# Performance work log

Hardware: AMD Instinct MI355X
Metric: run time of the kernel (lower is better)

Reference implementation:

```python
import jax, jax.numpy as jnp
import numpy as np

B, S, D, H = 4, 2048, 1024, 16
DH = D // H  # 64
R = 12       # random-projection rank forced by U's view()
EPS = 1e-6


def setup_inputs() -> dict:
    key = jax.random.key(0)
    ks = jax.random.split(key, 8)
    sc = 1.0 / np.sqrt(D)
    return {
        "Q": jax.random.normal(ks[0], (B, S, D), jnp.float32),
        "K": jax.random.normal(ks[1], (B, S, D), jnp.float32),
        "V": jax.random.normal(ks[2], (B, S, D), jnp.float32),
        "U": jax.random.normal(ks[3], (B, H, R, DH), jnp.float32),
        "W_Q": jax.random.normal(ks[4], (D, D), jnp.float32) * sc,
        "W_K": jax.random.normal(ks[5], (D, D), jnp.float32) * sc,
        "W_V": jax.random.normal(ks[6], (D, D), jnp.float32) * sc,
        "W_lin": jax.random.normal(ks[7], (D, D), jnp.float32) * sc,
        "b_lin": jnp.zeros((D,), jnp.float32),
        "gamma": jnp.ones((D,), jnp.float32),
        "beta": jnp.zeros((D,), jnp.float32),
    }


def reference(Q, K, V, U, W_Q, W_K, W_V, W_lin, b_lin, gamma, beta):
    b, s, d_model = Q.shape

    def proj(X, W):  # nn.Linear (no bias): X @ W^T, split heads -> [B,H,S,dh]
        return (X @ W.T).reshape(b, s, H, DH).transpose(0, 2, 1, 3)

    q = proj(Q, W_Q)
    k = proj(K, W_K)
    v = proj(V, W_V)

    # scores = (q @ U^T)^T @ k : random projection onto R=12 dims
    s1 = jnp.einsum('bhsd,bhrd->bhsr', q, U)          # [B,H,S,R]
    s2 = jnp.einsum('bhsr,bhsd->bhrd', s1, k)         # [B,H,R,dh]
    attn = jax.nn.softmax(s2, axis=-1)                # softmax over dh
    ctx = jnp.einsum('bhrd,bhsd->bhrs', attn, v)      # [B,H,R,S]
    # transpose(1,2) -> [B,R,H,S], flatten to [B, R*H*S/D, D]
    ctx = ctx.transpose(0, 2, 1, 3).reshape(b, -1, d_model)

    out = ctx @ W_lin.T + b_lin                       # final linear
    # dropout is identity in eval mode; then LayerNorm(eps=1e-6)
    mu = jnp.mean(out, axis=-1, keepdims=True)
    var = jnp.var(out, axis=-1, keepdims=True)
    return (out - mu) * jax.lax.rsqrt(var + EPS) * gamma + beta
```

## Files before the change

kernel.cpp:

```cpp
#include <hip/hip_runtime.h>

#define NB 4
#define NS 2048
#define ND 1024
#define NH 16
#define NDH 64
#define NR 12
#define NRH 192

typedef __attribute__((ext_vector_type(8))) short bf16x8;
typedef __attribute__((ext_vector_type(4))) float f32x4;

__device__ __forceinline__ unsigned short rnbf(float f) {
  unsigned u = __float_as_uint(f);
  u += 0x7fffu + ((u >> 16) & 1u);
  return (unsigned short)(u >> 16);
}
__device__ __forceinline__ float bf2f(unsigned short h) {
  return __uint_as_float(((unsigned)h) << 16);
}

__device__ __forceinline__ unsigned cvtpk(float a, float b) {
  unsigned r;
  asm("v_cvt_pk_bf16_f32 %0, %1, %2" : "=v"(r) : "v"(a), "v"(b));
  return r;
}
__device__ __forceinline__ uint4 pk_hi(float4 u, float4 w) {
  uint4 h;
  h.x = cvtpk(u.x, u.y); h.y = cvtpk(u.z, u.w);
  h.z = cvtpk(w.x, w.y); h.w = cvtpk(w.z, w.w);
  return h;
}
__device__ __forceinline__ unsigned lo2(float a, float b, unsigned hh) {
  float ah = __uint_as_float(hh << 16);
  float bh = __uint_as_float(hh & 0xffff0000u);
  return cvtpk(a - ah, b - bh);
}
__device__ __forceinline__ uint4 pk_lo(float4 u, float4 w, uint4 h) {
  uint4 l;
  l.x = lo2(u.x, u.y, h.x); l.y = lo2(u.z, u.w, h.y);
  l.z = lo2(w.x, w.y, h.z); l.w = lo2(w.z, w.w, h.w);
  return l;
}

__device__ __forceinline__ void gload16(const void* g, void* l) {
  __builtin_amdgcn_global_load_lds(
      (const __attribute__((address_space(1))) unsigned int*)g,
      (__attribute__((address_space(3))) unsigned int*)l, 16, 0, 0);
}

#define MFMA(a, b, c) __builtin_amdgcn_mfma_f32_16x16x32_bf16(a, b, c, 0, 0, 0)

__global__ __launch_bounds__(256) void build_wqeff(const float* __restrict__ U,
                                                   const float* __restrict__ WQ,
                                                   unsigned short* __restrict__ wqhi,
                                                   unsigned short* __restrict__ wqlo) {
  int idx = blockIdx.x;
  int hr = idx % (NH * NR);
  int h = hr / NR;
  __shared__ float u[NDH];
  int t = threadIdx.x;
  if (t < NDH) u[t] = U[(size_t)idx * NDH + t];
  __syncthreads();
  int e0 = t * 4;
  float a0 = 0.f, a1 = 0.f, a2 = 0.f, a3 = 0.f;
  const float* wbase = WQ + (size_t)h * NDH * ND + e0;
#pragma unroll 4
  for (int d = 0; d < NDH; ++d) {
    float uv = u[d];
    const float* wr = wbase + (size_t)d * ND;
    a0 += uv * wr[0]; a1 += uv * wr[1]; a2 += uv * wr[2]; a3 += uv * wr[3];
  }
  ushort4 h4, l4;
  h4.x = rnbf(a0); l4.x = rnbf(a0 - bf2f(h4.x));
  h4.y = rnbf(a1); l4.y = rnbf(a1 - bf2f(h4.y));
  h4.z = rnbf(a2); l4.z = rnbf(a2 - bf2f(h4.z));
  h4.w = rnbf(a3); l4.w = rnbf(a3 - bf2f(h4.w));
  *(ushort4*)&wqhi[(size_t)idx * ND + e0] = h4;
  *(ushort4*)&wqlo[(size_t)idx * ND + e0] = l4;
}

template <bool PAIR>
__global__ __launch_bounds__(256) void gemm_tn(
    const float* __restrict__ Af,
    const unsigned short* __restrict__ Bhi, const unsigned short* __restrict__ Blo,
    unsigned short* __restrict__ C0, unsigned short* __restrict__ C1) {
  constexpr int NBUF = PAIR ? 2 : 1;
  __shared__ unsigned short As[2][NBUF][32 * 64];
  __shared__ unsigned short Bs[2][NBUF][64 * 64];
  const int tid = threadIdx.x;
  const int lane = tid & 63;
  const int wid = tid >> 6;
  const int wm = wid >> 1, wn = wid & 1;

  int lin = blockIdx.x;
  int xcd = lin & 7, slot = lin >> 3;
  int b = slot / 24;
  int rem = slot % 24;
  int m0 = ((rem / 3) * 8 + xcd) * 32;
  int n0 = (rem % 3) * 64;

  const float* pA = Af + (size_t)b * NS * ND;
  const unsigned short* pBhi = Bhi + (size_t)b * NRH * ND;
  const unsigned short* pBlo = PAIR ? Blo + (size_t)b * NRH * ND : nullptr;

  const int rsub = lane >> 3;
  const int slotg = (lane & 7) ^ rsub;
  const int arow = tid >> 3;
  const int jg = tid & 7;

  f32x4 acc[2];
  acc[0] = (f32x4){0.f, 0.f, 0.f, 0.f};
  acc[1] = (f32x4){0.f, 0.f, 0.f, 0.f};

  {
    const float* asrc = pA + (size_t)(m0 + arow) * ND + jg * 8;
    float4 au = *(const float4*)(asrc);
    float4 av = *(const float4*)(asrc + 4);
#pragma unroll
    for (int cc = 0; cc < 2; ++cc) {
      int c = wid * 2 + cc;
      int grow = n0 + c * 8 + rsub;
      gload16(&pBhi[(size_t)grow * ND + slotg * 8], &Bs[0][0][c * 512]);
      if (PAIR)
        gload16(&pBlo[(size_t)grow * ND + slotg * 8], &Bs[0][NBUF - 1][c * 512]);
    }
    uint4 h = pk_hi(au, av);
    char* dst = (char*)&As[0][0][0] + arow * 128 + ((jg ^ (arow & 7)) << 4);
    *(uint4*)dst = h;
    if (PAIR) *(uint4*)(dst + 4096) = pk_lo(au, av, h);
  }
  __syncthreads();

  int p = 0;
  for (int k0 = 0; k0 < ND; k0 += 64, p ^= 1) {
    const bool pre = (k0 + 64) < ND;
    float4 aun = {}, avn = {};
    if (pre) {
      const float* asrc = pA + (size_t)(m0 + arow) * ND + k0 + 64 + jg * 8;
      aun = *(const float4*)(asrc);
      avn = *(const float4*)(asrc + 4);
#pragma unroll
      for (int cc = 0; cc < 2; ++cc) {
        int c = wid * 2 + cc;
        int grow = n0 + c * 8 + rsub;
        gload16(&pBhi[(size_t)grow * ND + k0 + 64 + slotg * 8],
                &Bs[p ^ 1][0][c * 512]);
        if (PAIR)
          gload16(&pBlo[(size_t)grow * ND + k0 + 64 + slotg * 8],
                  &Bs[p ^ 1][NBUF - 1][c * 512]);
      }
    }
#pragma unroll
    for (int kk = 0; kk < 64; kk += 32) {
      int sig = (kk >> 3) + (lane >> 4);
      bf16x8 ah, al, bh[2], bl[2];
      {
        int r = wm * 16 + (lane & 15);
        int off = r * 128 + ((sig ^ (r & 7)) << 4);
        ah = *(const bf16x8*)((const char*)&As[p][0][0] + off);
        if (PAIR) al = *(const bf16x8*)((const char*)&As[p][NBUF - 1][0] + off);
      }
#pragma unroll
      for (int fn = 0; fn < 2; ++fn) {
        int r = wn * 32 + fn * 16 + (lane & 15);
        int off = r * 128 + ((sig ^ (r & 7)) << 4);
        bh[fn] = *(const bf16x8*)((const char*)&Bs[p][0][0] + off);
        if (PAIR)
          bl[fn] = *(const bf16x8*)((const char*)&Bs[p][NBUF - 1][0] + off);
      }
#pragma unroll
      for (int fn = 0; fn < 2; ++fn) {
        acc[fn] = MFMA(ah, bh[fn], acc[fn]);
        if (PAIR) {
          acc[fn] = MFMA(ah, bl[fn], acc[fn]);
          acc[fn] = MFMA(al, bh[fn], acc[fn]);
        }
      }
    }
    if (pre) {
      uint4 h = pk_hi(aun, avn);
      char* dst =
          (char*)&As[p ^ 1][0][0] + arow * 128 + ((jg ^ (arow & 7)) << 4);
      *(uint4*)dst = h;
      if (PAIR) *(uint4*)(dst + 4096) = pk_lo(aun, avn, h);
    }
    __syncthreads();
  }

  const int jr = lane >> 4, cl = lane & 15;
#pragma unroll
  for (int fn = 0; fn < 2; ++fn) {
    f32x4 v = acc[fn];
    int s = m0 + wm * 16 + jr * 4;
    int rh = n0 + wn * 32 + fn * 16 + cl;
    int orow = PAIR ? rh : (rh % NR) * NH + rh / NR;
    size_t o = ((size_t)b * NRH + orow) * NS + s;
    ushort4 h4;
    h4.x = rnbf(v[0]); h4.y = rnbf(v[1]);
    h4.z = rnbf(v[2]); h4.w = rnbf(v[3]);
    *(ushort4*)&C0[o] = h4;
    if (PAIR) {
      ushort4 l4;
      l4.x = rnbf(v[0] - bf2f(h4.x)); l4.y = rnbf(v[1] - bf2f(h4.y));
      l4.z = rnbf(v[2] - bf2f(h4.z)); l4.w = rnbf(v[3] - bf2f(h4.w));
      *(ushort4*)&C1[o] = l4;
    }
  }
}

__global__ __launch_bounds__(256) void gemm_g2(
    const unsigned short* __restrict__ Ahi, const unsigned short* __restrict__ Alo,
    const float* __restrict__ Kf, float* __restrict__ P,
    int kchunk, int nz) {
  __shared__ unsigned short As[2][64 * 64];
  __shared__ unsigned short Bs[2][64 * 64];
  __shared__ float tbuf[64 * 68];
  const int tid = threadIdx.x;
  const int lane = tid & 63;
  const int wid = tid >> 6;
  const int wm = wid >> 1, wn = wid & 1;

  int lin = blockIdx.x;
  int bz, m_idx, n_idx;
  if (nz == 16) {
    int xcd = lin & 7, slot = lin >> 3;
    bz = xcd + 8 * (slot / 48);
    int rem = slot % 48;
    m_idx = rem / 16; n_idx = rem % 16;
  } else {
    bz = lin / 48;
    int rem = lin % 48;
    m_idx = rem / 16; n_idx = rem % 16;
  }
  const int m0 = m_idx * 64, n0 = n_idx * 64;
  const int b = bz % NB;
  const int kbeg = (bz / NB) * kchunk;
  const unsigned short* pAhi = Ahi + (size_t)b * NRH * NS;
  const unsigned short* pAlo = Alo + (size_t)b * NRH * NS;
  const float* pK = Kf + (size_t)b * NS * ND;

  const int rsub = lane >> 3;
  const int slotg = (lane & 7) ^ rsub;
  const int sr = tid >> 2;
  const int eg = (tid & 3) * 16;

  f32x4 acc[2][2];
#pragma unroll
  for (int i = 0; i < 2; ++i)
#pragma unroll
    for (int j = 0; j < 2; ++j) acc[i][j] = (f32x4){0.f, 0.f, 0.f, 0.f};

  float4 kr0, kr1, kr2, kr3;
  {
    const float* ksrc = pK + (size_t)(kbeg + sr) * ND + n0 + eg;
    kr0 = *(const float4*)(ksrc + 0);
    kr1 = *(const float4*)(ksrc + 4);
    kr2 = *(const float4*)(ksrc + 8);
    kr3 = *(const float4*)(ksrc + 12);
  }

  for (int k0 = kbeg; k0 < kbeg + kchunk; k0 += 64) {
#pragma unroll
    for (int cc = 0; cc < 2; ++cc) {
      int c = wid * 2 + cc;
      int grow = m0 + c * 8 + rsub;
      gload16(&pAhi[(size_t)grow * NS + k0 + slotg * 8], &As[0][c * 512]);
      gload16(&pAlo[(size_t)grow * NS + k0 + slotg * 8], &As[1][c * 512]);
    }
    {
      float* td = &tbuf[sr * 68 + eg];
      *(float4*)(td + 0) = kr0;
      *(float4*)(td + 4) = kr1;
      *(float4*)(td + 8) = kr2;
      *(float4*)(td + 12) = kr3;
    }
    __syncthreads();
    {
      const int e = tid & 63;
      const int sg = (tid >> 6) * 16;
      float v[16];
#pragma unroll
      for (int i = 0; i < 16; ++i) v[i] = tbuf[(sg + i) * 68 + e];
      float4 u0 = {v[0], v[1], v[2], v[3]},   w0 = {v[4], v[5], v[6], v[7]};
      float4 u1 = {v[8], v[9], v[10], v[11]}, w1 = {v[12], v[13], v[14], v[15]};
      uint4 h0 = pk_hi(u0, w0), h1 = pk_hi(u1, w1);
      int j0 = sg >> 3;
      char* dbase = (char*)&Bs[0][0] + e * 128;
      *(uint4*)(dbase + (((j0 + 0) ^ (e & 7)) << 4)) = h0;
      *(uint4*)(dbase + (((j0 + 1) ^ (e & 7)) << 4)) = h1;
      char* dlo = (char*)&Bs[1][0] + e * 128;
      *(uint4*)(dlo + (((j0 + 0) ^ (e & 7)) << 4)) = pk_lo(u0, w0, h0);
      *(uint4*)(dlo + (((j0 + 1) ^ (e & 7)) << 4)) = pk_lo(u1, w1, h1);
    }
    __syncthreads();
    if (k0 + 64 < kbeg + kchunk) {
      const float* ksrc = pK + (size_t)(k0 + 64 + sr) * ND + n0 + eg;
      kr0 = *(const float4*)(ksrc + 0);
      kr1 = *(const float4*)(ksrc + 4);
      kr2 = *(const float4*)(ksrc + 8);
      kr3 = *(const float4*)(ksrc + 12);
    }
#pragma unroll
    for (int kk = 0; kk < 64; kk += 32) {
      int sig = (kk >> 3) + (lane >> 4);
      bf16x8 ah[2], al[2], bh[2], bl[2];
#pragma unroll
      for (int fm = 0; fm < 2; ++fm) {
        int r = wm * 32 + fm * 16 + (lane & 15);
        int off = r * 128 + ((sig ^ (r & 7)) << 4);
        ah[fm] = *(const bf16x8*)((const char*)&As[0][0] + off);
        al[fm] = *(const bf16x8*)((const char*)&As[1][0] + off);
      }
#pragma unroll
      for (int fn = 0; fn < 2; ++fn) {
        int r = wn * 32 + fn * 16 + (lane & 15);
        int off = r * 128 + ((sig ^ (r & 7)) << 4);
        bh[fn] = *(const bf16x8*)((const char*)&Bs[0][0] + off);
        bl[fn] = *(const bf16x8*)((const char*)&Bs[1][0] + off);
      }
#pragma unroll
      for (int fm = 0; fm < 2; ++fm)
#pragma unroll
        for (int fn = 0; fn < 2; ++fn) {
          acc[fm][fn] = MFMA(ah[fm], bh[fn], acc[fm][fn]);
          acc[fm][fn] = MFMA(ah[fm], bl[fn], acc[fm][fn]);
          acc[fm][fn] = MFMA(al[fm], bh[fn], acc[fm][fn]);
        }
    }
    __syncthreads();
  }

  const int jr = lane >> 4, cl = lane & 15;
  float* pc = P + (size_t)bz * NRH * ND;
#pragma unroll
  for (int fm = 0; fm < 2; ++fm)
#pragma unroll
    for (int fn = 0; fn < 2; ++fn) {
      f32x4 v = acc[fm][fn];
      int gcol = n0 + wn * 32 + fn * 16 + cl;
#pragma unroll
      for (int j = 0; j < 4; ++j) {
        int m = m0 + wm * 32 + fm * 16 + jr * 4 + j;
        pc[(size_t)m * ND + gcol] = v[j];
      }
    }
}

__global__ __launch_bounds__(256) void gemm_g4(
    const unsigned short* __restrict__ A, const float* __restrict__ Bf,
    float* __restrict__ lin) {
  __shared__ unsigned short As[2][64 * 64];
  __shared__ unsigned short Bs[2][64 * 64];
  const int tid = threadIdx.x;
  const int lane = tid & 63;
  const int wid = tid >> 6;
  const int wm = wid >> 1, wn = wid & 1;
  const int m0 = (blockIdx.x >> 4) * 64, n0 = (blockIdx.x & 15) * 64;
  const int rsub = lane >> 3;
  const int slotg = (lane & 7) ^ rsub;
  const int brow = tid >> 2;
  const int jbase = (tid & 3) * 2;

  f32x4 acc[2][2];
#pragma unroll
  for (int i = 0; i < 2; ++i)
#pragma unroll
    for (int j = 0; j < 2; ++j) acc[i][j] = (f32x4){0.f, 0.f, 0.f, 0.f};

#pragma unroll
  for (int cc = 0; cc < 2; ++cc) {
    int c = wid * 2 + cc;
    gload16(&A[(size_t)(m0 + c * 8 + rsub) * ND + slotg * 8], &As[0][c * 512]);
  }
  {
    const float* bsrc = Bf + (size_t)(n0 + brow) * ND + jbase * 8;
    float4 u0 = *(const float4*)(bsrc + 0), v0 = *(const float4*)(bsrc + 4);
    float4 u1 = *(const float4*)(bsrc + 8), v1 = *(const float4*)(bsrc + 12);
    char* dbase = (char*)&Bs[0][0] + brow * 128;
    *(uint4*)(dbase + (((jbase + 0) ^ (brow & 7)) << 4)) = pk_hi(u0, v0);
    *(uint4*)(dbase + (((jbase + 1) ^ (brow & 7)) << 4)) = pk_hi(u1, v1);
  }
  __syncthreads();

  int p = 0;
  for (int k0 = 0; k0 < ND; k0 += 64, p ^= 1) {
    const bool pre = (k0 + 64) < ND;
    float4 pu0 = {}, pv0 = {}, pu1 = {}, pv1 = {};
    if (pre) {
#pragma unroll
      for (int cc = 0; cc < 2; ++cc) {
        int c = wid * 2 + cc;
        gload16(&A[(size_t)(m0 + c * 8 + rsub) * ND + k0 + 64 + slotg * 8],
                &As[p ^ 1][c * 512]);
      }
      const float* bsrc = Bf + (size_t)(n0 + brow) * ND + k0 + 64 + jbase * 8;
      pu0 = *(const float4*)(bsrc + 0); pv0 = *(const float4*)(bsrc + 4);
      pu1 = *(const float4*)(bsrc + 8); pv1 = *(const float4*)(bsrc + 12);
    }
#pragma unroll
    for (int kk = 0; kk < 64; kk += 32) {
      int sig = (kk >> 3) + (lane >> 4);
      bf16x8 ah[2], bh[2];
#pragma unroll
      for (int fm = 0; fm < 2; ++fm) {
        int r = wm * 32 + fm * 16 + (lane & 15);
        int off = r * 128 + ((sig ^ (r & 7)) << 4);
        ah[fm] = *(const bf16x8*)((const char*)&As[p][0] + off);
      }
#pragma unroll
      for (int fn = 0; fn < 2; ++fn) {
        int r = wn * 32 + fn * 16 + (lane & 15);
        int off = r * 128 + ((sig ^ (r & 7)) << 4);
        bh[fn] = *(const bf16x8*)((const char*)&Bs[p][0] + off);
      }
#pragma unroll
      for (int fm = 0; fm < 2; ++fm)
#pragma unroll
        for (int fn = 0; fn < 2; ++fn)
          acc[fm][fn] = MFMA(ah[fm], bh[fn], acc[fm][fn]);
    }
    if (pre) {
      char* dbase = (char*)&Bs[p ^ 1][0] + brow * 128;
      *(uint4*)(dbase + (((jbase + 0) ^ (brow & 7)) << 4)) = pk_hi(pu0, pv0);
      *(uint4*)(dbase + (((jbase + 1) ^ (brow & 7)) << 4)) = pk_hi(pu1, pv1);
    }
    __syncthreads();
  }

  const int jr = lane >> 4, cl = lane & 15;
#pragma unroll
  for (int fm = 0; fm < 2; ++fm)
#pragma unroll
    for (int fn = 0; fn < 2; ++fn) {
      f32x4 v = acc[fm][fn];
      int gcol = n0 + wn * 32 + fn * 16 + cl;
#pragma unroll
      for (int j = 0; j < 4; ++j) {
        int m = m0 + wm * 32 + fm * 16 + jr * 4 + j;
        lin[(size_t)m * ND + gcol] = v[j];
      }
    }
}

__global__ __launch_bounds__(256) void bias_ln(const float* __restrict__ lin,
                                               const float* __restrict__ bias,
                                               const float* __restrict__ gamma,
                                               const float* __restrict__ beta,
                                               float* __restrict__ out) {
  int row = blockIdx.x;
  int t = threadIdx.x;
  float4 a = ((const float4*)(lin + (size_t)row * ND))[t];
  float4 bv = ((const float4*)bias)[t];
  a.x += bv.x; a.y += bv.y; a.z += bv.z; a.w += bv.w;

  float s = a.x + a.y + a.z + a.w;
  float ss = a.x * a.x + a.y * a.y + a.z * a.z + a.w * a.w;
#pragma unroll
  for (int off = 32; off > 0; off >>= 1) {
    s += __shfl_xor(s, off);
    ss += __shfl_xor(ss, off);
  }
  __shared__ float red[8];
  int wave = t >> 6, lane = t & 63;
  if (lane == 0) { red[wave] = s; red[4 + wave] = ss; }
  __syncthreads();
  s = red[0] + red[1] + red[2] + red[3];
  ss = red[4] + red[5] + red[6] + red[7];
  float mu = s * (1.0f / ND);
  float var = ss * (1.0f / ND) - mu * mu;
  float inv = rsqrtf(var + 1e-6f);
  float4 g = ((const float4*)gamma)[t];
  float4 be = ((const float4*)beta)[t];
  float4 o;
  o.x = (a.x - mu) * inv * g.x + be.x;
  o.y = (a.y - mu) * inv * g.y + be.y;
  o.z = (a.z - mu) * inv * g.z + be.z;
  o.w = (a.w - mu) * inv * g.w + be.w;
  ((float4*)(out + (size_t)row * ND))[t] = o;
}

__global__ __launch_bounds__(256) void sm_k(const float* __restrict__ P,
                                            int nsplit,
                                            const float* __restrict__ WK,
                                            const float* __restrict__ WV,
                                            unsigned short* __restrict__ A2) {
  int x = blockIdx.x;
  int xcd = x & 7, within = x >> 3;
  int h = xcd + 8 * (within & 1);
  int rb = within >> 1;
  int r = rb >> 2, b = rb & 3;
  int idx = (b * NH + h) * NR + r;
  int rh = h * NR + r;

  const int t = threadIdx.x;
  const int lane = t & 63, wv = t >> 6;
  __shared__ float t1s[ND];
  __shared__ float s2s[NDH];
  __shared__ float attns[NDH];

  {
    const size_t sstride = (size_t)NB * NRH * ND;
    const float* base = P + ((size_t)b * NRH + rh) * ND;
    float4 a = ((const float4*)base)[t];
    for (int s = 1; s < nsplit; ++s) {
      float4 v = ((const float4*)(base + (size_t)s * sstride))[t];
      a.x += v.x; a.y += v.y; a.z += v.z; a.w += v.w;
    }
    ((float4*)t1s)[t] = a;
  }
  __syncthreads();

  for (int j = 0; j < 16; ++j) {
    int d = wv * 16 + j;
    const float* row = WK + (size_t)(h * NDH + d) * ND;
    float acc = 0.f;
#pragma unroll
    for (int i = 0; i < 16; ++i) acc += row[lane + i * 64] * t1s[lane + i * 64];
#pragma unroll
    for (int off = 32; off > 0; off >>= 1) acc += __shfl_xor(acc, off);
    if (lane == 0) s2s[d] = acc;
  }
  __syncthreads();

  if (t < NDH) {
    float s2 = s2s[t];
    float m = s2;
#pragma unroll
    for (int off = 32; off > 0; off >>= 1) m = fmaxf(m, __shfl_xor(m, off));
    float e = __expf(s2 - m);
    float sum = e;
#pragma unroll
    for (int off = 32; off > 0; off >>= 1) sum += __shfl_xor(sum, off);
    attns[t] = e / sum;
  }
  __syncthreads();

  {
    int e0 = t * 4;
    const float* wvp = WV + (size_t)h * NDH * ND + e0;
    float a0 = 0.f, a1 = 0.f, a2 = 0.f, a3 = 0.f;
#pragma unroll 4
    for (int dd = 0; dd < NDH; ++dd) {
      float4 wvv = *(const float4*)&wvp[(size_t)dd * ND];
      float a = attns[dd];
      a0 += a * wvv.x; a1 += a * wvv.y; a2 += a * wvv.z; a3 += a * wvv.w;
    }
    ushort4 o;
    o.x = rnbf(a0); o.y = rnbf(a1); o.z = rnbf(a2); o.w = rnbf(a3);
    *(ushort4*)&A2[(size_t)idx * ND + e0] = o;
  }
}

extern "C" void kernel_launch(void* const* d_in, const int* in_sizes, int n_in,
                              void* d_out, int out_size, void* d_ws, size_t ws_size,
                              hipStream_t stream) {
  const float* Q = (const float*)d_in[0];
  const float* K = (const float*)d_in[1];
  const float* V = (const float*)d_in[2];
  const float* U = (const float*)d_in[3];
  const float* WQ = (const float*)d_in[4];
  const float* WK = (const float*)d_in[5];
  const float* WV = (const float*)d_in[6];
  const float* WL = (const float*)d_in[7];
  const float* bl = (const float*)d_in[8];
  const float* ga = (const float*)d_in[9];
  const float* be = (const float*)d_in[10];
  float* out = (float*)d_out;
  char* w = (char*)d_ws;

  unsigned short* wqhi = (unsigned short*)w;
  unsigned short* wqlo = (unsigned short*)(w + 1572864);
  unsigned short* A2b = wqhi;
  unsigned short* s1hi = (unsigned short*)(w + 3145728);
  unsigned short* s1lo = (unsigned short*)(w + 6291456);
  unsigned short* ctxb = (unsigned short*)(w + 9437184);
  float* lin = (float*)(w + 12582912);
  float* P = (float*)(w + 18874368);

  size_t avail = ws_size > 18874368 ? ws_size - 18874368 : 0;
  int sG2 = 1;
  while (sG2 * 2 <= 4 && 3145728ull * (size_t)(sG2 * 2) <= avail) sG2 *= 2;

  build_wqeff<<<NB * NH * NR, 256, 0, stream>>>(U, WQ, wqhi, wqlo);

  gemm_tn<true><<<768, 256, 0, stream>>>(Q, wqhi, wqlo, s1hi, s1lo);

  gemm_g2<<<48 * NB * sG2, 256, 0, stream>>>(s1hi, s1lo, K, P, 2048 / sG2,
                                             NB * sG2);

  sm_k<<<NB * NH * NR, 256, 0, stream>>>(P, sG2, WK, WV, A2b);

  gemm_tn<false><<<768, 256, 0, stream>>>(V, A2b, nullptr, ctxb, nullptr);

  gemm_g4<<<384, 256, 0, stream>>>(ctxb, WL, lin);

  bias_ln<<<NB * 384, 256, 0, stream>>>(lin, bl, ga, be, out);
}
```

Measured before the change: 107.7 us.

## Halve GEMM M-tiles and drop LDS double buffering to double grid size

The Q/V projection GEMMs (gemm_tn) shrink their M tile from 32 to 16 rows and the output GEMM (gemm_g4) from 64 to 32 rows, doubling the launch grids. Both kernels drop the register-prefetch/LDS double-buffer pipeline for a single-buffer load, sync, compute, sync loop. The aim is more blocks and less LDS per block for better occupancy and wave coverage across CUs. The cost is that global-load latency is no longer hidden behind MFMA work, B tiles are re-read more often, and there is an odd `&As[0][0] == nullptr ? nullptr : ...` destination expression.

```diff
diff --git a/kernel.cpp b/kernel.cpp
--- a/kernel.cpp
+++ b/kernel.cpp
@@ -86,18 +86,17 @@
     const unsigned short* __restrict__ Bhi, const unsigned short* __restrict__ Blo,
     unsigned short* __restrict__ C0, unsigned short* __restrict__ C1) {
   constexpr int NBUF = PAIR ? 2 : 1;
-  __shared__ unsigned short As[2][NBUF][32 * 64];
-  __shared__ unsigned short Bs[2][NBUF][64 * 64];
+  __shared__ unsigned short As[NBUF][16 * 64];
+  __shared__ unsigned short Bs[NBUF][64 * 64];
   const int tid = threadIdx.x;
   const int lane = tid & 63;
   const int wid = tid >> 6;
-  const int wm = wid >> 1, wn = wid & 1;
 
   int lin = blockIdx.x;
   int xcd = lin & 7, slot = lin >> 3;
-  int b = slot / 24;
-  int rem = slot % 24;
-  int m0 = ((rem / 3) * 8 + xcd) * 32;
+  int b = slot / 48;
+  int rem = slot % 48;
+  int m0 = ((rem / 3) * 8 + xcd) * 16;
   int n0 = (rem % 3) * 64;
 
   const float* pA = Af + (size_t)b * NS * ND;
@@ -106,104 +105,75 @@
 
   const int rsub = lane >> 3;
   const int slotg = (lane & 7) ^ rsub;
-  const int arow = tid >> 3;
-  const int jg = tid & 7;
-
-  f32x4 acc[2];
-  acc[0] = (f32x4){0.f, 0.f, 0.f, 0.f};
-  acc[1] = (f32x4){0.f, 0.f, 0.f, 0.f};
-
-  {
-    const float* asrc = pA + (size_t)(m0 + arow) * ND + jg * 8;
-    float4 au = *(const float4*)(asrc);
-    float4 av = *(const float4*)(asrc + 4);
+  const int arow = tid >> 4;
+  const int aj = (tid & 15) >> 1;
+  const int ah8 = (tid & 1) * 8;
+
+  f32x4 acc = (f32x4){0.f, 0.f, 0.f, 0.f};
+
+  for (int k0 = 0; k0 < ND; k0 += 64) {
+    {
+      const float* asrc = pA + (size_t)(m0 + arow) * ND + k0 + (tid & 15) * 4;
+      float4 v = *(const float4*)asrc;
+      uint2 h;
+      h.x = cvtpk(v.x, v.y); h.y = cvtpk(v.z, v.w);
+      char* dst = (char*)&As[0][0] + arow * 128 + ((aj ^ (arow & 7)) << 4) + ah8;
+      *(uint2*)dst = h;
+      if (PAIR) {
+        uint2 l;
+        l.x = lo2(v.x, v.y, h.x); l.y = lo2(v.z, v.w, h.y);
+        *(uint2*)(dst + 2048) = l;
+      }
+    }
 #pragma unroll
     for (int cc = 0; cc < 2; ++cc) {
       int c = wid * 2 + cc;
       int grow = n0 + c * 8 + rsub;
-      gload16(&pBhi[(size_t)grow * ND + slotg * 8], &Bs[0][0][c * 512]);
+      gload16(&pBhi[(size_t)grow * ND + k0 + slotg * 8], &As[0][0] == nullptr ? nullptr : &Bs[0][c * 512]);
       if (PAIR)
-        gload16(&pBlo[(size_t)grow * ND + slotg * 8], &Bs[0][NBUF - 1][c * 512]);
-    }
-    uint4 h = pk_hi(au, av);
-    char* dst = (char*)&As[0][0][0] + arow * 128 + ((jg ^ (arow & 7)) << 4);
-    *(uint4*)dst = h;
-    if (PAIR) *(uint4*)(dst + 4096) = pk_lo(au, av, h);
-  }
-  __syncthreads();
-
-  int p = 0;
-  for (int k0 = 0; k0 < ND; k0 += 64, p ^= 1) {
-    const bool pre = (k0 + 64) < ND;
-    float4 aun = {}, avn = {};
-    if (pre) {
-      const float* asrc = pA + (size_t)(m0 + arow) * ND + k0 + 64 + jg * 8;
-      aun = *(const float4*)(asrc);
-      avn = *(const float4*)(asrc + 4);
-#pragma unroll
-      for (int cc = 0; cc < 2; ++cc) {
-        int c = wid * 2 + cc;
-        int grow = n0 + c * 8 + rsub;
-        gload16(&pBhi[(size_t)grow * ND + k0 + 64 + slotg * 8],
-                &Bs[p ^ 1][0][c * 512]);
-        if (PAIR)
-          gload16(&pBlo[(size_t)grow * ND + k0 + 64 + slotg * 8],
-                  &Bs[p ^ 1][NBUF - 1][c * 512]);
-      }
-    }
+        gload16(&pBlo[(size_t)grow * ND + k0 + slotg * 8], &Bs[NBUF - 1][c * 512]);
+    }
+    __syncthreads();
+
 #pragma unroll
     for (int kk = 0; kk < 64; kk += 32) {
       int sig = (kk >> 3) + (lane >> 4);
-      bf16x8 ah, al, bh[2], bl[2];
+      bf16x8 ah, al, bh, bl;
       {
-        int r = wm * 16 + (lane & 15);
+        int r = lane & 15;
         int off = r * 128 + ((sig ^ (r & 7)) << 4);
-        ah = *(const bf16x8*)((const char*)&As[p][0][0] + off);
-        if (PAIR) al = *(const bf16x8*)((const char*)&As[p][NBUF - 1][0] + off);
-      }
-#pragma unroll
-      for (int fn = 0; fn < 2; ++fn) {
-        int r = wn * 32 + fn * 16 + (lane & 15);
+        ah = *(const bf16x8*)((const char*)&As[0][0] + off);
+        if (PAIR) al = *(const bf16x8*)((const char*)&As[0][0] + 2048 + off);
+      }
+      {
+        int r = wid * 16 + (lane & 15);
         int off = r * 128 + ((sig ^ (r & 7)) << 4);
-        bh[fn] = *(const bf16x8*)((const char*)&Bs[p][0][0] + off);
-        if (PAIR)
-          bl[fn] = *(const bf16x8*)((const char*)&Bs[p][NBUF - 1][0] + off);
-      }
-#pragma unroll
-      for (int fn = 0; fn < 2; ++fn) {
-        acc[fn] = MFMA(ah, bh[fn], acc[fn]);
-        if (PAIR) {
-          acc[fn] = MFMA(ah, bl[fn], acc[fn]);
-          acc[fn] = MFMA(al, bh[fn], acc[fn]);
-        }
-      }
-    }
-    if (pre) {
-      uint4 h = pk_hi(aun, avn);
-      char* dst =
-          (char*)&As[p ^ 1][0][0] + arow * 128 + ((jg ^ (arow & 7)) << 4);
-      *(uint4*)dst = h;
-      if (PAIR) *(uint4*)(dst + 4096) = pk_lo(aun, avn, h);
+        bh = *(const bf16x8*)((const char*)&Bs[0][0] + off);
+        if (PAIR) bl = *(const bf16x8*)((const char*)&Bs[0][0] + 8192 + off);
+      }
+      acc = MFMA(ah, bh, acc);
+      if (PAIR) {
+        acc = MFMA(ah, bl, acc);
+        acc = MFMA(al, bh, acc);
+      }
     }
     __syncthreads();
   }
 
   const int jr = lane >> 4, cl = lane & 15;
-#pragma unroll
-  for (int fn = 0; fn < 2; ++fn) {
-    f32x4 v = acc[fn];
-    int s = m0 + wm * 16 + jr * 4;
-    int rh = n0 + wn * 32 + fn * 16 + cl;
+  {
+    int s = m0 + jr * 4;
+    int rh = n0 + wid * 16 + cl;
     int orow = PAIR ? rh : (rh % NR) * NH + rh / NR;
     size_t o = ((size_t)b * NRH + orow) * NS + s;
     ushort4 h4;
-    h4.x = rnbf(v[0]); h4.y = rnbf(v[1]);
-    h4.z = rnbf(v[2]); h4.w = rnbf(v[3]);
+    h4.x = rnbf(acc[0]); h4.y = rnbf(acc[1]);
+    h4.z = rnbf(acc[2]); h4.w = rnbf(acc[3]);
     *(ushort4*)&C0[o] = h4;
     if (PAIR) {
       ushort4 l4;
-      l4.x = rnbf(v[0] - bf2f(h4.x)); l4.y = rnbf(v[1] - bf2f(h4.y));
-      l4.z = rnbf(v[2] - bf2f(h4.z)); l4.w = rnbf(v[3] - bf2f(h4.w));
+      l4.x = rnbf(acc[0] - bf2f(h4.x)); l4.y = rnbf(acc[1] - bf2f(h4.y));
+      l4.z = rnbf(acc[2] - bf2f(h4.z)); l4.w = rnbf(acc[3] - bf2f(h4.w));
       *(ushort4*)&C1[o] = l4;
     }
   }
@@ -350,97 +320,67 @@
 __global__ __launch_bounds__(256) void gemm_g4(
     const unsigned short* __restrict__ A, const float* __restrict__ Bf,
     float* __restrict__ lin) {
-  __shared__ unsigned short As[2][64 * 64];
-  __shared__ unsigned short Bs[2][64 * 64];
+  __shared__ unsigned short As[32 * 64];
+  __shared__ unsigned short Bs[64 * 64];
   const int tid = threadIdx.x;
   const int lane = tid & 63;
   const int wid = tid >> 6;
   const int wm = wid >> 1, wn = wid & 1;
-  const int m0 = (blockIdx.x >> 4) * 64, n0 = (blockIdx.x & 15) * 64;
+  const int m0 = (blockIdx.x >> 4) * 32, n0 = (blockIdx.x & 15) * 64;
   const int rsub = lane >> 3;
   const int slotg = (lane & 7) ^ rsub;
   const int brow = tid >> 2;
   const int jbase = (tid & 3) * 2;
 
-  f32x4 acc[2][2];
-#pragma unroll
-  for (int i = 0; i < 2; ++i)
-#pragma unroll
-    for (int j = 0; j < 2; ++j) acc[i][j] = (f32x4){0.f, 0.f, 0.f, 0.f};
-
-#pragma unroll
-  for (int cc = 0; cc < 2; ++cc) {
-    int c = wid * 2 + cc;
-    gload16(&A[(size_t)(m0 + c * 8 + rsub) * ND + slotg * 8], &As[0][c * 512]);
-  }
-  {
-    const float* bsrc = Bf + (size_t)(n0 + brow) * ND + jbase * 8;
-    float4 u0 = *(const float4*)(bsrc + 0), v0 = *(const float4*)(bsrc + 4);
-    float4 u1 = *(const float4*)(bsrc + 8), v1 = *(const float4*)(bsrc + 12);
-    char* dbase = (char*)&Bs[0][0] + brow * 128;
-    *(uint4*)(dbase + (((jbase + 0) ^ (brow & 7)) << 4)) = pk_hi(u0, v0);
-    *(uint4*)(dbase + (((jbase + 1) ^ (brow & 7)) << 4)) = pk_hi(u1, v1);
-  }
-  __syncthreads();
-
-  int p = 0;
-  for (int k0 = 0; k0 < ND; k0 += 64, p ^= 1) {
-    const bool pre = (k0 + 64) < ND;
-    float4 pu0 = {}, pv0 = {}, pu1 = {}, pv1 = {};
-    if (pre) {
-#pragma unroll
-      for (int cc = 0; cc < 2; ++cc) {
-        int c = wid * 2 + cc;
-        gload16(&A[(size_t)(m0 + c * 8 + rsub) * ND + k0 + 64 + slotg * 8],
-                &As[p ^ 1][c * 512]);
-      }
-      const float* bsrc = Bf + (size_t)(n0 + brow) * ND + k0 + 64 + jbase * 8;
-      pu0 = *(const float4*)(bsrc + 0); pv0 = *(const float4*)(bsrc + 4);
-      pu1 = *(const float4*)(bsrc + 8); pv1 = *(const float4*)(bsrc + 12);
-    }
+  f32x4 acc[2];
+  acc[0] = (f32x4){0.f, 0.f, 0.f, 0.f};
+  acc[1] = (f32x4){0.f, 0.f, 0.f, 0.f};
+
+  for (int k0 = 0; k0 < ND; k0 += 64) {
+    gload16(&A[(size_t)(m0 + wid * 8 + rsub) * ND + k0 + slotg * 8],
+            &As[wid * 512]);
+    {
+      const float* bsrc = Bf + (size_t)(n0 + brow) * ND + k0 + jbase * 8;
+      float4 u0 = *(const float4*)(bsrc + 0), v0 = *(const float4*)(bsrc + 4);
+      float4 u1 = *(const float4*)(bsrc + 8), v1 = *(const float4*)(bsrc + 12);
+      char* dbase = (char*)&Bs[0] + brow * 128;
+      *(uint4*)(dbase + (((jbase + 0) ^ (brow & 7)) << 4)) = pk_hi(u0, v0);
+      *(uint4*)(dbase + (((jbase + 1) ^ (brow & 7)) << 4)) = pk_hi(u1, v1);
+    }
+    __syncthreads();
+
 #pragma unroll
     for (int kk = 0; kk < 64; kk += 32) {
       int sig = (kk >> 3) + (lane >> 4);
-      bf16x8 ah[2], bh[2];
-#pragma unroll
-      for (int fm = 0; fm < 2; ++fm) {
-        int r = wm * 32 + fm * 16 + (lane & 15);
+      bf16x8 ah, bh[2];
+      {
+        int r = wm * 16 + (lane & 15);
         int off = r * 128 + ((sig ^ (r & 7)) << 4);
-        ah[fm] = *(const bf16x8*)((const char*)&As[p][0] + off);
+        ah = *(const bf16x8*)((const char*)&As[0] + off);
       }
 #pragma unroll
       for (int fn = 0; fn < 2; ++fn) {
         int r = wn * 32 + fn * 16 + (lane & 15);
         int off = r * 128 + ((sig ^ (r & 7)) << 4);
-        bh[fn] = *(const bf16x8*)((const char*)&Bs[p][0] + off);
-      }
-#pragma unroll
-      for (int fm = 0; fm < 2; ++fm)
-#pragma unroll
-        for (int fn = 0; fn < 2; ++fn)
-          acc[fm][fn] = MFMA(ah[fm], bh[fn], acc[fm][fn]);
-    }
-    if (pre) {
-      char* dbase = (char*)&Bs[p ^ 1][0] + brow * 128;
-      *(uint4*)(dbase + (((jbase + 0) ^ (brow & 7)) << 4)) = pk_hi(pu0, pv0);
-      *(uint4*)(dbase + (((jbase + 1) ^ (brow & 7)) << 4)) = pk_hi(pu1, pv1);
+        bh[fn] = *(const bf16x8*)((const char*)&Bs[0] + off);
+      }
+#pragma unroll
+      for (int fn = 0; fn < 2; ++fn) acc[fn] = MFMA(ah, bh[fn], acc[fn]);
     }
     __syncthreads();
   }
 
   const int jr = lane >> 4, cl = lane & 15;
 #pragma unroll
-  for (int fm = 0; fm < 2; ++fm)
-#pragma unroll
-    for (int fn = 0; fn < 2; ++fn) {
-      f32x4 v = acc[fm][fn];
-      int gcol = n0 + wn * 32 + fn * 16 + cl;
-#pragma unroll
-      for (int j = 0; j < 4; ++j) {
-        int m = m0 + wm * 32 + fm * 16 + jr * 4 + j;
-        lin[(size_t)m * ND + gcol] = v[j];
-      }
-    }
+  for (int fn = 0; fn < 2; ++fn) {
+    f32x4 v = acc[fn];
+    int gcol = n0 + wn * 32 + fn * 16 + cl;
+#pragma unroll
+    for (int j = 0; j < 4; ++j) {
+      int m = m0 + wm * 16 + jr * 4 + j;
+      lin[(size_t)m * ND + gcol] = v[j];
+    }
+  }
 }
 
 __global__ __launch_bounds__(256) void bias_ln(const float* __restrict__ lin,
@@ -584,16 +524,16 @@
 
   build_wqeff<<<NB * NH * NR, 256, 0, stream>>>(U, WQ, wqhi, wqlo);
 
-  gemm_tn<true><<<768, 256, 0, stream>>>(Q, wqhi, wqlo, s1hi, s1lo);
+  gemm_tn<true><<<1536, 256, 0, stream>>>(Q, wqhi, wqlo, s1hi, s1lo);
 
   gemm_g2<<<48 * NB * sG2, 256, 0, stream>>>(s1hi, s1lo, K, P, 2048 / sG2,
                                              NB * sG2);
 
   sm_k<<<NB * NH * NR, 256, 0, stream>>>(P, sG2, WK, WV, A2b);
 
-  gemm_tn<false><<<768, 256, 0, stream>>>(V, A2b, nullptr, ctxb, nullptr);
-
-  gemm_g4<<<384, 256, 0, stream>>>(ctxb, WL, lin);
+  gemm_tn<false><<<1536, 256, 0, stream>>>(V, A2b, nullptr, ctxb, nullptr);
+
+  gemm_g4<<<768, 256, 0, stream>>>(ctxb, WL, lin);
 
   bias_ln<<<NB * 384, 256, 0, stream>>>(lin, bl, ga, be, out);
 }
```

New measurement: 115.3 us. +7.0%, slower.

## Enlarge gemm_tn tiles to 64x64 with 128-wide K steps, drop double buffering

Applied to the files above, without the earlier changes.

gemm_tn now computes 64x64 output tiles per block with a 2x2 MFMA fragment grid per wave and stages 128-wide K slices, halving the grid to 384 blocks. The aim is more reuse of each A and B fragment loaded from LDS and half as many loop iterations and barriers. The register-prefetch double buffering is removed, so global loads no longer overlap with MFMA work inside a block. Occupancy also drops because LDS per block grows and the grid is smaller.

```diff
diff --git a/kernel.cpp b/kernel.cpp
--- a/kernel.cpp
+++ b/kernel.cpp
@@ -86,8 +86,9 @@
     const unsigned short* __restrict__ Bhi, const unsigned short* __restrict__ Blo,
     unsigned short* __restrict__ C0, unsigned short* __restrict__ C1) {
   constexpr int NBUF = PAIR ? 2 : 1;
-  __shared__ unsigned short As[2][NBUF][32 * 64];
-  __shared__ unsigned short Bs[2][NBUF][64 * 64];
+  constexpr int PLANE = 64 * 128 * 2;
+  __shared__ unsigned short As[NBUF][64 * 128];
+  __shared__ unsigned short Bs[NBUF][64 * 128];
   const int tid = threadIdx.x;
   const int lane = tid & 63;
   const int wid = tid >> 6;
@@ -95,118 +96,102 @@
 
   int lin = blockIdx.x;
   int xcd = lin & 7, slot = lin >> 3;
-  int b = slot / 24;
-  int rem = slot % 24;
-  int m0 = ((rem / 3) * 8 + xcd) * 32;
+  int b = slot / 12;
+  int rem = slot % 12;
+  int m0 = ((rem / 3) * 8 + xcd) * 64;
   int n0 = (rem % 3) * 64;
 
   const float* pA = Af + (size_t)b * NS * ND;
   const unsigned short* pBhi = Bhi + (size_t)b * NRH * ND;
   const unsigned short* pBlo = PAIR ? Blo + (size_t)b * NRH * ND : nullptr;
 
-  const int rsub = lane >> 3;
-  const int slotg = (lane & 7) ^ rsub;
-  const int arow = tid >> 3;
-  const int jg = tid & 7;
-
-  f32x4 acc[2];
-  acc[0] = (f32x4){0.f, 0.f, 0.f, 0.f};
-  acc[1] = (f32x4){0.f, 0.f, 0.f, 0.f};
-
-  {
-    const float* asrc = pA + (size_t)(m0 + arow) * ND + jg * 8;
-    float4 au = *(const float4*)(asrc);
-    float4 av = *(const float4*)(asrc + 4);
-#pragma unroll
-    for (int cc = 0; cc < 2; ++cc) {
-      int c = wid * 2 + cc;
-      int grow = n0 + c * 8 + rsub;
-      gload16(&pBhi[(size_t)grow * ND + slotg * 8], &Bs[0][0][c * 512]);
-      if (PAIR)
-        gload16(&pBlo[(size_t)grow * ND + slotg * 8], &Bs[0][NBUF - 1][c * 512]);
-    }
-    uint4 h = pk_hi(au, av);
-    char* dst = (char*)&As[0][0][0] + arow * 128 + ((jg ^ (arow & 7)) << 4);
-    *(uint4*)dst = h;
-    if (PAIR) *(uint4*)(dst + 4096) = pk_lo(au, av, h);
-  }
-  __syncthreads();
-
-  int p = 0;
-  for (int k0 = 0; k0 < ND; k0 += 64, p ^= 1) {
-    const bool pre = (k0 + 64) < ND;
-    float4 aun = {}, avn = {};
-    if (pre) {
-      const float* asrc = pA + (size_t)(m0 + arow) * ND + k0 + 64 + jg * 8;
-      aun = *(const float4*)(asrc);
-      avn = *(const float4*)(asrc + 4);
-#pragma unroll
-      for (int cc = 0; cc < 2; ++cc) {
-        int c = wid * 2 + cc;
-        int grow = n0 + c * 8 + rsub;
-        gload16(&pBhi[(size_t)grow * ND + k0 + 64 + slotg * 8],
-                &Bs[p ^ 1][0][c * 512]);
-        if (PAIR)
-          gload16(&pBlo[(size_t)grow * ND + k0 + 64 + slotg * 8],
-                  &Bs[p ^ 1][NBUF - 1][c * 512]);
-      }
-    }
-#pragma unroll
-    for (int kk = 0; kk < 64; kk += 32) {
+  const int arow = tid >> 2;
+  const int aq = (tid & 3) * 4;
+
+  f32x4 acc[2][2];
+#pragma unroll
+  for (int i = 0; i < 2; ++i)
+#pragma unroll
+    for (int j = 0; j < 2; ++j) acc[i][j] = (f32x4){0.f, 0.f, 0.f, 0.f};
+
+  for (int k0 = 0; k0 < ND; k0 += 128) {
+#pragma unroll
+    for (int cc = 0; cc < 4; ++cc) {
+      int c = wid * 4 + cc;
+      int lrow = c * 4 + (lane >> 4);
+      int sslot = (lane & 15) ^ (lrow & 7);
+      size_t gaddr = (size_t)(n0 + lrow) * ND + k0 + sslot * 8;
+      gload16(&pBhi[gaddr], (char*)&Bs[0][0] + c * 1024);
+      if (PAIR) gload16(&pBlo[gaddr], (char*)&Bs[NBUF - 1][0] + c * 1024);
+    }
+    {
+      const float* asrc = pA + (size_t)(m0 + arow) * ND + k0 + aq * 8;
+      char* abase = (char*)&As[0][0] + arow * 256;
+#pragma unroll
+      for (int jj = 0; jj < 4; ++jj) {
+        float4 u = *(const float4*)(asrc + jj * 8);
+        float4 v = *(const float4*)(asrc + jj * 8 + 4);
+        uint4 h = pk_hi(u, v);
+        char* dst = abase + (((aq + jj) ^ (arow & 7)) << 4);
+        *(uint4*)dst = h;
+        if (PAIR) *(uint4*)(dst + PLANE) = pk_lo(u, v, h);
+      }
+    }
+    __syncthreads();
+
+#pragma unroll
+    for (int kk = 0; kk < 128; kk += 32) {
       int sig = (kk >> 3) + (lane >> 4);
-      bf16x8 ah, al, bh[2], bl[2];
-      {
-        int r = wm * 16 + (lane & 15);
-        int off = r * 128 + ((sig ^ (r & 7)) << 4);
-        ah = *(const bf16x8*)((const char*)&As[p][0][0] + off);
-        if (PAIR) al = *(const bf16x8*)((const char*)&As[p][NBUF - 1][0] + off);
+      bf16x8 ah[2], al[2], bh[2], bl[2];
+#pragma unroll
+      for (int fm = 0; fm < 2; ++fm) {
+        int r = wm * 32 + fm * 16 + (lane & 15);
+        int off = r * 256 + ((sig ^ (r & 7)) << 4);
+        ah[fm] = *(const bf16x8*)((const char*)&As[0][0] + off);
+        if (PAIR) al[fm] = *(const bf16x8*)((const char*)&As[0][0] + PLANE + off);
       }
 #pragma unroll
       for (int fn = 0; fn < 2; ++fn) {
         int r = wn * 32 + fn * 16 + (lane & 15);
-        int off = r * 128 + ((sig ^ (r & 7)) << 4);
-        bh[fn] = *(const bf16x8*)((const char*)&Bs[p][0][0] + off);
-        if (PAIR)
-          bl[fn] = *(const bf16x8*)((const char*)&Bs[p][NBUF - 1][0] + off);
-      }
-#pragma unroll
-      for (int fn = 0; fn < 2; ++fn) {
-        acc[fn] = MFMA(ah, bh[fn], acc[fn]);
-        if (PAIR) {
-          acc[fn] = MFMA(ah, bl[fn], acc[fn]);
-          acc[fn] = MFMA(al, bh[fn], acc[fn]);
+        int off = r * 256 + ((sig ^ (r & 7)) << 4);
+        bh[fn] = *(const bf16x8*)((const char*)&Bs[0][0] + off);
+        if (PAIR) bl[fn] = *(const bf16x8*)((const char*)&Bs[0][0] + PLANE + off);
+      }
+#pragma unroll
+      for (int fm = 0; fm < 2; ++fm)
+#pragma unroll
+        for (int fn = 0; fn < 2; ++fn) {
+          acc[fm][fn] = MFMA(ah[fm], bh[fn], acc[fm][fn]);
+          if (PAIR) {
+            acc[fm][fn] = MFMA(ah[fm], bl[fn], acc[fm][fn]);
+            acc[fm][fn] = MFMA(al[fm], bh[fn], acc[fm][fn]);
+          }
         }
-      }
-    }
-    if (pre) {
-      uint4 h = pk_hi(aun, avn);
-      char* dst =
-          (char*)&As[p ^ 1][0][0] + arow * 128 + ((jg ^ (arow & 7)) << 4);
-      *(uint4*)dst = h;
-      if (PAIR) *(uint4*)(dst + 4096) = pk_lo(aun, avn, h);
     }
     __syncthreads();
   }
 
   const int jr = lane >> 4, cl = lane & 15;
 #pragma unroll
-  for (int fn = 0; fn < 2; ++fn) {
-    f32x4 v = acc[fn];
-    int s = m0 + wm * 16 + jr * 4;
-    int rh = n0 + wn * 32 + fn * 16 + cl;
-    int orow = PAIR ? rh : (rh % NR) * NH + rh / NR;
-    size_t o = ((size_t)b * NRH + orow) * NS + s;
-    ushort4 h4;
-    h4.x = rnbf(v[0]); h4.y = rnbf(v[1]);
-    h4.z = rnbf(v[2]); h4.w = rnbf(v[3]);
-    *(ushort4*)&C0[o] = h4;
-    if (PAIR) {
-      ushort4 l4;
-      l4.x = rnbf(v[0] - bf2f(h4.x)); l4.y = rnbf(v[1] - bf2f(h4.y));
-      l4.z = rnbf(v[2] - bf2f(h4.z)); l4.w = rnbf(v[3] - bf2f(h4.w));
-      *(ushort4*)&C1[o] = l4;
-    }
-  }
+  for (int fm = 0; fm < 2; ++fm)
+#pragma unroll
+    for (int fn = 0; fn < 2; ++fn) {
+      f32x4 v = acc[fm][fn];
+      int s = m0 + wm * 32 + fm * 16 + jr * 4;
+      int rh = n0 + wn * 32 + fn * 16 + cl;
+      int orow = PAIR ? rh : (rh % NR) * NH + rh / NR;
+      size_t o = ((size_t)b * NRH + orow) * NS + s;
+      ushort4 h4;
+      h4.x = rnbf(v[0]); h4.y = rnbf(v[1]);
+      h4.z = rnbf(v[2]); h4.w = rnbf(v[3]);
+      *(ushort4*)&C0[o] = h4;
+      if (PAIR) {
+        ushort4 l4;
+        l4.x = rnbf(v[0] - bf2f(h4.x)); l4.y = rnbf(v[1] - bf2f(h4.y));
+        l4.z = rnbf(v[2] - bf2f(h4.z)); l4.w = rnbf(v[3] - bf2f(h4.w));
+        *(ushort4*)&C1[o] = l4;
+      }
+    }
 }
 
 __global__ __launch_bounds__(256) void gemm_g2(
@@ -584,14 +569,14 @@
 
   build_wqeff<<<NB * NH * NR, 256, 0, stream>>>(U, WQ, wqhi, wqlo);
 
-  gemm_tn<true><<<768, 256, 0, stream>>>(Q, wqhi, wqlo, s1hi, s1lo);
+  gemm_tn<true><<<384, 256, 0, stream>>>(Q, wqhi, wqlo, s1hi, s1lo);
 
   gemm_g2<<<48 * NB * sG2, 256, 0, stream>>>(s1hi, s1lo, K, P, 2048 / sG2,
                                              NB * sG2);
 
   sm_k<<<NB * NH * NR, 256, 0, stream>>>(P, sG2, WK, WV, A2b);
 
-  gemm_tn<false><<<768, 256, 0, stream>>>(V, A2b, nullptr, ctxb, nullptr);
+  gemm_tn<false><<<384, 256, 0, stream>>>(V, A2b, nullptr, ctxb, nullptr);
 
   gemm_g4<<<384, 256, 0, stream>>>(ctxb, WL, lin);
 
```

After: 123.3 us. +14.5%, slower.

## Batch six projection ranks per block in softmax kernel to reuse WK/WV rows

Applied to the files above, without the earlier changes.

The softmax kernel used to run one block per (batch, head, rank), so it reloaded the head's 64x1024 WK and WV slices 12 times per head. It now runs 128 blocks of 512 threads. Each block handles six ranks of one head, keeps each WK row in registers across the six dot products, and reuses each WV float4 load for three ranks. This cuts redundant global and L2 traffic for the weights, at the cost of fewer blocks (128 on a large GPU), more LDS per block and more registers.

```diff
diff --git a/kernel.cpp b/kernel.cpp
--- a/kernel.cpp
+++ b/kernel.cpp
@@ -480,75 +480,97 @@
   ((float4*)(out + (size_t)row * ND))[t] = o;
 }
 
-__global__ __launch_bounds__(256) void sm_k(const float* __restrict__ P,
-                                            int nsplit,
-                                            const float* __restrict__ WK,
-                                            const float* __restrict__ WV,
-                                            unsigned short* __restrict__ A2) {
+__global__ __launch_bounds__(512) void sm_k2(const float* __restrict__ P,
+                                             int nsplit,
+                                             const float* __restrict__ WK,
+                                             const float* __restrict__ WV,
+                                             unsigned short* __restrict__ A2) {
   int x = blockIdx.x;
-  int xcd = x & 7, within = x >> 3;
-  int h = xcd + 8 * (within & 1);
-  int rb = within >> 1;
-  int r = rb >> 2, b = rb & 3;
-  int idx = (b * NH + h) * NR + r;
-  int rh = h * NR + r;
+  int h = (x & 7) + 8 * ((x >> 3) & 1);
+  int rhalf = (x >> 4) & 1;
+  int b = x >> 5;
 
   const int t = threadIdx.x;
   const int lane = t & 63, wv = t >> 6;
-  __shared__ float t1s[ND];
-  __shared__ float s2s[NDH];
-  __shared__ float attns[NDH];
+  __shared__ float t1s[6][ND];
+  __shared__ float s2s[6][NDH];
+  __shared__ float attns[6][NDH];
 
   {
     const size_t sstride = (size_t)NB * NRH * ND;
-    const float* base = P + ((size_t)b * NRH + rh) * ND;
-    float4 a = ((const float4*)base)[t];
-    for (int s = 1; s < nsplit; ++s) {
-      float4 v = ((const float4*)(base + (size_t)s * sstride))[t];
-      a.x += v.x; a.y += v.y; a.z += v.z; a.w += v.w;
-    }
-    ((float4*)t1s)[t] = a;
+    for (int i = t; i < 6 * 256; i += 512) {
+      int rr = i >> 8;
+      int c4 = i & 255;
+      int rh = h * NR + rhalf * 6 + rr;
+      const float* base = P + ((size_t)b * NRH + rh) * ND;
+      float4 a = ((const float4*)base)[c4];
+      for (int s = 1; s < nsplit; ++s) {
+        float4 v = ((const float4*)(base + (size_t)s * sstride))[c4];
+        a.x += v.x; a.y += v.y; a.z += v.z; a.w += v.w;
+      }
+      ((float4*)t1s[rr])[c4] = a;
+    }
   }
   __syncthreads();
 
-  for (int j = 0; j < 16; ++j) {
-    int d = wv * 16 + j;
+  for (int j = 0; j < 8; ++j) {
+    int d = wv * 8 + j;
     const float* row = WK + (size_t)(h * NDH + d) * ND;
-    float acc = 0.f;
-#pragma unroll
-    for (int i = 0; i < 16; ++i) acc += row[lane + i * 64] * t1s[lane + i * 64];
-#pragma unroll
-    for (int off = 32; off > 0; off >>= 1) acc += __shfl_xor(acc, off);
-    if (lane == 0) s2s[d] = acc;
+    float rw[16];
+#pragma unroll
+    for (int i = 0; i < 16; ++i) rw[i] = row[lane + i * 64];
+#pragma unroll
+    for (int rr = 0; rr < 6; ++rr) {
+      float acc = 0.f;
+#pragma unroll
+      for (int i = 0; i < 16; ++i) acc += rw[i] * t1s[rr][lane + i * 64];
+#pragma unroll
+      for (int off = 32; off > 0; off >>= 1) acc += __shfl_xor(acc, off);
+      if (lane == 0) s2s[rr][d] = acc;
+    }
   }
   __syncthreads();
 
-  if (t < NDH) {
-    float s2 = s2s[t];
-    float m = s2;
+  if (wv < 6) {
+    float v = s2s[wv][lane];
+    float m = v;
 #pragma unroll
     for (int off = 32; off > 0; off >>= 1) m = fmaxf(m, __shfl_xor(m, off));
-    float e = __expf(s2 - m);
+    float e = __expf(v - m);
     float sum = e;
 #pragma unroll
     for (int off = 32; off > 0; off >>= 1) sum += __shfl_xor(sum, off);
-    attns[t] = e / sum;
+    attns[wv][lane] = e / sum;
   }
   __syncthreads();
 
   {
-    int e0 = t * 4;
+    int e0 = (t & 255) * 4;
+    int rg = t >> 8;
     const float* wvp = WV + (size_t)h * NDH * ND + e0;
-    float a0 = 0.f, a1 = 0.f, a2 = 0.f, a3 = 0.f;
+    float acc[3][4];
+#pragma unroll
+    for (int q = 0; q < 3; ++q) {
+      acc[q][0] = 0.f; acc[q][1] = 0.f; acc[q][2] = 0.f; acc[q][3] = 0.f;
+    }
 #pragma unroll 4
     for (int dd = 0; dd < NDH; ++dd) {
-      float4 wvv = *(const float4*)&wvp[(size_t)dd * ND];
-      float a = attns[dd];
-      a0 += a * wvv.x; a1 += a * wvv.y; a2 += a * wvv.z; a3 += a * wvv.w;
-    }
-    ushort4 o;
-    o.x = rnbf(a0); o.y = rnbf(a1); o.z = rnbf(a2); o.w = rnbf(a3);
-    *(ushort4*)&A2[(size_t)idx * ND + e0] = o;
+      float4 w4 = *(const float4*)&wvp[(size_t)dd * ND];
+#pragma unroll
+      for (int q = 0; q < 3; ++q) {
+        float a = attns[rg * 3 + q][dd];
+        acc[q][0] += a * w4.x; acc[q][1] += a * w4.y;
+        acc[q][2] += a * w4.z; acc[q][3] += a * w4.w;
+      }
+    }
+#pragma unroll
+    for (int q = 0; q < 3; ++q) {
+      int idx = (b * NH + h) * NR + rhalf * 6 + rg * 3 + q;
+      ushort4 o;
+      o.x = rnbf(acc[q][0]); o.y = rnbf(acc[q][1]);
+      o.z = rnbf(acc[q][2]); o.w = rnbf(acc[q][3]);
+      *(ushort4*)&A2[(size_t)idx * ND + e0] = o;
+    }
   }
 }
 
@@ -589,7 +611,7 @@
   gemm_g2<<<48 * NB * sG2, 256, 0, stream>>>(s1hi, s1lo, K, P, 2048 / sG2,
                                              NB * sG2);
 
-  sm_k<<<NB * NH * NR, 256, 0, stream>>>(P, sG2, WK, WV, A2b);
+  sm_k2<<<128, 512, 0, stream>>>(P, sG2, WK, WV, A2b);
 
   gemm_tn<false><<<768, 256, 0, stream>>>(V, A2b, nullptr, ctxb, nullptr);
 
```

Measured after the change: 114.2 us. 1.06x slower.
